# Performance work log

Measured on AMD Instinct MI355X. Metric: run time of the kernel, lower is better.

The kernel has to match this reference:

```python
import jax, jax.numpy as jnp
import numpy as np
from jax import lax

N_LAYER = 2
D_MODEL = 256
D_INNER = 512   # expand * d_model
D_STATE = 16
DT_RANK = 16    # ceil(d_model / 16)
D_CONV = 4
VOCAB = 256
B, L = 4, 2048


def setup_inputs() -> dict:
    key = jax.random.key(0)
    ks = jax.random.split(key, 12)
    s = 0.02
    embedding = jax.random.normal(ks[0], (VOCAB, D_MODEL), jnp.float32) * s
    in_proj_w = jax.random.normal(ks[1], (N_LAYER, D_MODEL, 2 * D_INNER), jnp.float32) * s
    conv_w = jax.random.normal(ks[2], (N_LAYER, D_INNER, 1, D_CONV), jnp.float32) * 0.1
    conv_b = jax.random.normal(ks[3], (N_LAYER, D_INNER), jnp.float32) * 0.01
    x_proj_w = jax.random.normal(ks[4], (N_LAYER, D_INNER, DT_RANK + 2 * D_STATE), jnp.float32) * s
    dt_proj_w = jax.random.normal(ks[5], (N_LAYER, DT_RANK, D_INNER), jnp.float32) * (DT_RANK ** -0.5)
    dt_proj_b = jax.random.normal(ks[6], (N_LAYER, D_INNER), jnp.float32) * 0.1
    # S4D-real init: A = -[1..d_state], stored as A_log
    A_log = jnp.log(jnp.broadcast_to(jnp.arange(1, D_STATE + 1, dtype=jnp.float32), (N_LAYER, D_INNER, D_STATE)))
    D = jnp.ones((N_LAYER, D_INNER), jnp.float32)
    out_proj_w = jax.random.normal(ks[7], (N_LAYER, D_INNER, D_MODEL), jnp.float32) * s
    input_ids = jax.random.randint(ks[8], (B, L), 0, VOCAB)
    return {"input_ids": input_ids, "embedding": embedding, "in_proj_w": in_proj_w,
            "conv_w": conv_w, "conv_b": conv_b, "x_proj_w": x_proj_w,
            "dt_proj_w": dt_proj_w, "dt_proj_b": dt_proj_b, "A_log": A_log,
            "D": D, "out_proj_w": out_proj_w}


def _selective_scan(u, delta, A, Bc, Cc):
    # u, delta: [B, L, d_inner]; A: [d_inner, N]; Bc, Cc: [B, L, N]
    def step(h, inp):
        d_t, b_t, c_t, u_t = inp  # [B,d_inner], [B,N], [B,N], [B,d_inner]
        dA = jnp.exp(d_t[:, :, None] * A)                    # [B, d_inner, N]
        h = dA * h + (d_t * u_t)[:, :, None] * b_t[:, None, :]
        y = jnp.sum(h * c_t[:, None, :], axis=-1)            # [B, d_inner]
        return h, y

    h0 = jnp.zeros((u.shape[0], u.shape[2], A.shape[1]), u.dtype)
    xs = (jnp.moveaxis(delta, 1, 0), jnp.moveaxis(Bc, 1, 0),
          jnp.moveaxis(Cc, 1, 0), jnp.moveaxis(u, 1, 0))
    _, ys = lax.scan(step, h0, xs)  # ys: [L, B, d_inner]
    return jnp.moveaxis(ys, 0, 1)


def _mamba_block(x, w_in, w_conv, b_conv, w_xp, w_dt, b_dt, A_log, Dp, w_out):
    # x: [B, L, d_model]
    xz = x @ w_in                                            # [B, L, 2*d_inner]
    u, res = jnp.split(xz, 2, axis=-1)
    # depthwise causal conv1d
    uc = jnp.transpose(u, (0, 2, 1))                          # [B, d_inner, L]
    uc = lax.conv_general_dilated(uc, w_conv, window_strides=(1,),
                                  padding=[(D_CONV - 1, 0)],
                                  feature_group_count=D_INNER,
                                  dimension_numbers=("NCH", "OIH", "NCH"))
    uc = uc + b_conv[None, :, None]
    u = jax.nn.silu(jnp.transpose(uc, (0, 2, 1)))             # [B, L, d_inner]
    x_dbl = u @ w_xp                                          # [B, L, dt_rank + 2N]
    dt, Bc, Cc = jnp.split(x_dbl, [DT_RANK, DT_RANK + D_STATE], axis=-1)
    delta = jax.nn.softplus(dt @ w_dt + b_dt)                 # [B, L, d_inner]
    A = -jnp.exp(A_log)                                       # [d_inner, N]
    y = _selective_scan(u, delta, A, Bc, Cc) + u * Dp
    y = y * jax.nn.silu(res)
    return y @ w_out                                          # [B, L, d_model]


def reference(input_ids, embedding, in_proj_w, conv_w, conv_b, x_proj_w,
              dt_proj_w, dt_proj_b, A_log, D, out_proj_w):
    x = embedding[input_ids]                                  # [B, L, d_model]
    for l in range(N_LAYER):
        x = _mamba_block(x, in_proj_w[l], conv_w[l], conv_b[l], x_proj_w[l],
                         dt_proj_w[l], dt_proj_b[l], A_log[l], D[l], out_proj_w[l])
    return x
```

## Files before the change

kernel.cpp:

```cpp
#include <hip/hip_runtime.h>
#include <math.h>

#define NLAYER 2
#define DMODEL 256
#define DINNER 512
#define DSTATE 16
#define DTRANK 16
#define DCONV  4
#define BB     4
#define LL     2048
#define BL     (BB*LL)
#define NCHUNK 64
#define LC     (LL/NCHUNK)
#define NREC   (BB*DINNER*DSTATE)

typedef __attribute__((ext_vector_type(8))) short short8;
typedef __attribute__((ext_vector_type(4))) float f32x4;

__device__ __forceinline__ float sigmoidf_(float x) { return 1.0f / (1.0f + __expf(-x)); }

__device__ __forceinline__ unsigned f2bf(float a) {
    unsigned u = __builtin_bit_cast(unsigned, a);
    return (u + 0x7fffu + ((u >> 16) & 1u)) >> 16;
}
__device__ __forceinline__ float bf2f(unsigned h) {
    return __builtin_bit_cast(float, h << 16);
}

template<int K, bool EMB>
__global__ __launch_bounds__(256) void k_cvt_a(const float* __restrict__ A,
                                               ushort* __restrict__ F,
                                               const int* __restrict__ ids,
                                               const float* __restrict__ emb) {
    constexpr int NKF = K / 32;
    const int t = blockIdx.x * 256 + threadIdx.x;
    const int l = t & 63;
    const int cid = t >> 6;
    const int kf = cid % NKF;
    const int mf = cid / NKF;
    const int row = mf * 16 + (l & 15);
    const int k0 = kf * 32 + (l >> 4) * 8;
    const float* src = EMB ? &emb[(size_t)ids[row] * K + k0]
                           : &A[(size_t)row * K + k0];
    float4 v0 = *(const float4*)&src[0];
    float4 v1 = *(const float4*)&src[4];
    float s[8] = {v0.x, v0.y, v0.z, v0.w, v1.x, v1.y, v1.z, v1.w};
    unsigned hi[8], lo[8];
#pragma unroll
    for (int j = 0; j < 8; ++j) {
        hi[j] = f2bf(s[j]);
        lo[j] = f2bf(s[j] - bf2f(hi[j]));
    }
    uint4 ph = make_uint4(hi[0] | (hi[1] << 16), hi[2] | (hi[3] << 16),
                          hi[4] | (hi[5] << 16), hi[6] | (hi[7] << 16));
    uint4 pl = make_uint4(lo[0] | (lo[1] << 16), lo[2] | (lo[3] << 16),
                          lo[4] | (lo[5] << 16), lo[6] | (lo[7] << 16));
    size_t ohi = ((size_t)mf * (2 * NKF) + kf) * 512 + l * 8;
    *(uint4*)&F[ohi] = ph;
    *(uint4*)&F[ohi + (size_t)NKF * 512] = pl;
}

template<int K>
__global__ __launch_bounds__(256) void k_cvt_w(const float* __restrict__ W,
                                               ushort* __restrict__ F, int N) {
    constexpr int NKF = K / 32;
    const int t = blockIdx.x * 256 + threadIdx.x;
    const int l = t & 63;
    const int cid = t >> 6;
    const int kf = cid % NKF;
    const int nf = cid / NKF;
    const int col = nf * 16 + (l & 15);
    const int k0 = kf * 32 + (l >> 4) * 8;
    float s[8];
#pragma unroll
    for (int j = 0; j < 8; ++j) s[j] = W[(size_t)(k0 + j) * N + col];
    unsigned hi[8], lo[8];
#pragma unroll
    for (int j = 0; j < 8; ++j) {
        hi[j] = f2bf(s[j]);
        lo[j] = f2bf(s[j] - bf2f(hi[j]));
    }
    uint4 ph = make_uint4(hi[0] | (hi[1] << 16), hi[2] | (hi[3] << 16),
                          hi[4] | (hi[5] << 16), hi[6] | (hi[7] << 16));
    uint4 pl = make_uint4(lo[0] | (lo[1] << 16), lo[2] | (lo[3] << 16),
                          lo[4] | (lo[5] << 16), lo[6] | (lo[7] << 16));
    size_t ohi = ((size_t)nf * (2 * NKF) + kf) * 512 + l * 8;
    *(uint4*)&F[ohi] = ph;
    *(uint4*)&F[ohi + (size_t)NKF * 512] = pl;
}

template<int SPLITK>
__global__ __launch_bounds__(256) void k_mgemm(const ushort* __restrict__ Af,
                                               const ushort* __restrict__ Bf,
                                               float* __restrict__ C,
                                               int M, int N, int KE) {
    __shared__ __align__(16) ushort As[8 * 512];
    __shared__ __align__(16) ushort Bs[8 * 512];
    const int tid = threadIdx.x;
    const int w = tid >> 6, lane = tid & 63;
    const int n0 = blockIdx.x * 128, m0 = blockIdx.y * 128;
    const int nkf = KE >> 5;
    const int KT = nkf / SPLITK;
    const int kt0 = blockIdx.z * KT;
    const int wm = w & 1, wn = w >> 1;
    const int c0 = 2 * w, c1 = c0 + 1;

    f32x4 acc[4][4] = {};

    const ushort* Ab0 = Af + ((size_t)(m0 / 16 + c0) * nkf) * 512 + lane * 8;
    const ushort* Ab1 = Af + ((size_t)(m0 / 16 + c1) * nkf) * 512 + lane * 8;
    const ushort* Bb0 = Bf + ((size_t)(n0 / 16 + c0) * nkf) * 512 + lane * 8;
    const ushort* Bb1 = Bf + ((size_t)(n0 / 16 + c1) * nkf) * 512 + lane * 8;
    ushort* As0 = As + c0 * 512 + lane * 8;
    ushort* As1 = As + c1 * 512 + lane * 8;
    ushort* Bs0 = Bs + c0 * 512 + lane * 8;
    ushort* Bs1 = Bs + c1 * 512 + lane * 8;

    for (int kt = kt0; kt < kt0 + KT; ++kt) {
        const size_t ko = (size_t)kt * 512;
        __builtin_amdgcn_global_load_lds((const __attribute__((address_space(1))) void*)(Ab0 + ko),
                                         (__attribute__((address_space(3))) void*)As0, 16, 0, 0);
        __builtin_amdgcn_global_load_lds((const __attribute__((address_space(1))) void*)(Ab1 + ko),
                                         (__attribute__((address_space(3))) void*)As1, 16, 0, 0);
        __builtin_amdgcn_global_load_lds((const __attribute__((address_space(1))) void*)(Bb0 + ko),
                                         (__attribute__((address_space(3))) void*)Bs0, 16, 0, 0);
        __builtin_amdgcn_global_load_lds((const __attribute__((address_space(1))) void*)(Bb1 + ko),
                                         (__attribute__((address_space(3))) void*)Bs1, 16, 0, 0);
        __syncthreads();
        short8 av[4], bv[4];
#pragma unroll
        for (int i = 0; i < 4; ++i)
            av[i] = *(const short8*)&As[(wm * 4 + i) * 512 + lane * 8];
#pragma unroll
        for (int i = 0; i < 4; ++i)
            bv[i] = *(const short8*)&Bs[(wn * 4 + i) * 512 + lane * 8];
#pragma unroll
        for (int mi = 0; mi < 4; ++mi)
#pragma unroll
            for (int ni = 0; ni < 4; ++ni)
                acc[mi][ni] = __builtin_amdgcn_mfma_f32_16x16x32_bf16(av[mi], bv[ni],
                                                                      acc[mi][ni], 0, 0, 0);
        __syncthreads();
    }

    float* Cw = C + (size_t)blockIdx.z * ((size_t)M * N);
    const int r0 = (lane >> 4) * 4, cc = lane & 15;
#pragma unroll
    for (int mi = 0; mi < 4; ++mi)
#pragma unroll
        for (int r = 0; r < 4; ++r) {
            const int row = m0 + wm * 64 + mi * 16 + r0 + r;
            float* crow = &Cw[(size_t)row * N + n0 + wn * 64 + cc];
#pragma unroll
            for (int ni = 0; ni < 4; ++ni) crow[ni * 16] = acc[mi][ni][r];
        }
}

__global__ __launch_bounds__(256) void k_red4(const float* __restrict__ p,
                                              float* __restrict__ o, int n4) {
    int i = blockIdx.x * 256 + threadIdx.x;
    const float4* p4 = (const float4*)p;
    float4 a = p4[i], b = p4[i + n4], c = p4[i + 2 * n4], d = p4[i + 3 * n4];
    ((float4*)o)[i] = make_float4(a.x + b.x + c.x + d.x, a.y + b.y + c.y + d.y,
                                  a.z + b.z + c.z + d.z, a.w + b.w + c.w + d.w);
}

__global__ void k_conv_silu(const float* __restrict__ xz, const float* __restrict__ cw,
                            const float* __restrict__ cb, float* __restrict__ u) {
    int idx = blockIdx.x * blockDim.x + threadIdx.x;
    int c  = idx & (DINNER - 1);
    int bl = idx >> 9;
    int l  = bl & (LL - 1);
    float acc = cb[c];
#pragma unroll
    for (int k = 0; k < DCONV; ++k) {
        int t = l - (DCONV - 1) + k;
        if (t >= 0) acc += cw[c * DCONV + k] * xz[(size_t)(bl - (DCONV - 1) + k) * 2 * DINNER + c];
    }
    u[(size_t)idx] = acc * sigmoidf_(acc);
}

__global__ __launch_bounds__(256) void k_xpd(const float* __restrict__ u,
                                             const float* __restrict__ w_xp,
                                             const float* __restrict__ w_dt,
                                             const float* __restrict__ b_dt,
                                             float* __restrict__ Bm,
                                             float* __restrict__ Cm,
                                             float* __restrict__ delta) {
    const int tid = threadIdx.x;
    const int bl0 = blockIdx.x * 16;
    __shared__ float us[16 * DINNER];
    __shared__ float wsx[128 * 48];
    __shared__ float dts[16][DTRANK];

    {
        const float4* u4 = (const float4*)&u[(size_t)bl0 * DINNER];
        float4* us4 = (float4*)us;
#pragma unroll
        for (int q = 0; q < 8; ++q) us4[tid + q * 256] = u4[tid + q * 256];
    }

    const int mp = tid >> 5;
    const int jg = (tid >> 3) & 3;
    const int s  = tid & 7;
    const float* usm0 = &us[(mp * 2 + 0) * DINNER];
    const float* usm1 = &us[(mp * 2 + 1) * DINNER];

    float acc0[12] = {}, acc1[12] = {};
#pragma unroll 1
    for (int ck = 0; ck < 4; ++ck) {
        __syncthreads();
        {
            const float4* wg = (const float4*)&w_xp[ck * 128 * 48];
            float4* wl = (float4*)wsx;
#pragma unroll
            for (int q = 0; q < 6; ++q) wl[tid + q * 256] = wg[tid + q * 256];
        }
        __syncthreads();
#pragma unroll
        for (int i = 0; i < 16; ++i) {
            const int kl = i * 8 + s;
            const float a0 = usm0[ck * 128 + kl];
            const float a1 = usm1[ck * 128 + kl];
            const float* wr = &wsx[kl * 48 + jg * 12];
            float4 w0 = *(const float4*)&wr[0];
            float4 w1 = *(const float4*)&wr[4];
            float4 w2 = *(const float4*)&wr[8];
            acc0[0]  = fmaf(a0, w0.x, acc0[0]);  acc1[0]  = fmaf(a1, w0.x, acc1[0]);
            acc0[1]  = fmaf(a0, w0.y, acc0[1]);  acc1[1]  = fmaf(a1, w0.y, acc1[1]);
            acc0[2]  = fmaf(a0, w0.z, acc0[2]);  acc1[2]  = fmaf(a1, w0.z, acc1[2]);
            acc0[3]  = fmaf(a0, w0.w, acc0[3]);  acc1[3]  = fmaf(a1, w0.w, acc1[3]);
            acc0[4]  = fmaf(a0, w1.x, acc0[4]);  acc1[4]  = fmaf(a1, w1.x, acc1[4]);
            acc0[5]  = fmaf(a0, w1.y, acc0[5]);  acc1[5]  = fmaf(a1, w1.y, acc1[5]);
            acc0[6]  = fmaf(a0, w1.z, acc0[6]);  acc1[6]  = fmaf(a1, w1.z, acc1[6]);
            acc0[7]  = fmaf(a0, w1.w, acc0[7]);  acc1[7]  = fmaf(a1, w1.w, acc1[7]);
            acc0[8]  = fmaf(a0, w2.x, acc0[8]);  acc1[8]  = fmaf(a1, w2.x, acc1[8]);
            acc0[9]  = fmaf(a0, w2.y, acc0[9]);  acc1[9]  = fmaf(a1, w2.y, acc1[9]);
            acc0[10] = fmaf(a0, w2.z, acc0[10]); acc1[10] = fmaf(a1, w2.z, acc1[10]);
            acc0[11] = fmaf(a0, w2.w, acc0[11]); acc1[11] = fmaf(a1, w2.w, acc1[11]);
        }
    }
#pragma unroll
    for (int off = 4; off >= 1; off >>= 1) {
#pragma unroll
        for (int j = 0; j < 12; ++j) {
            acc0[j] += __shfl_xor(acc0[j], off, 8);
            acc1[j] += __shfl_xor(acc1[j], off, 8);
        }
    }
    if (s < 6) {
        const int bl_a = bl0 + mp * 2 + 0;
        const int bl_b = bl0 + mp * 2 + 1;
#pragma unroll
        for (int q = 0; q < 2; ++q) {
            int j = jg * 12 + s * 2 + q;
            float v0 = acc0[s * 2 + q];
            float v1 = acc1[s * 2 + q];
            if (j < 16) {
                dts[mp * 2 + 0][j] = v0;
                dts[mp * 2 + 1][j] = v1;
            } else if (j < 32) {
                Bm[(size_t)bl_a * DSTATE + (j - 16)] = v0;
                Bm[(size_t)bl_b * DSTATE + (j - 16)] = v1;
            } else {
                Cm[(size_t)bl_a * DSTATE + (j - 32)] = v0;
                Cm[(size_t)bl_b * DSTATE + (j - 32)] = v1;
            }
        }
    }
    __syncthreads();

    const int c0 = (tid & 127) * 4;
    const int mb = (tid >> 7) * 8;
    float4 bd = *(const float4*)&b_dt[c0];
    float a0[8], a1[8], a2[8], a3[8];
#pragma unroll
    for (int t = 0; t < 8; ++t) { a0[t] = bd.x; a1[t] = bd.y; a2[t] = bd.z; a3[t] = bd.w; }
#pragma unroll
    for (int r = 0; r < DTRANK; ++r) {
        float4 w4 = *(const float4*)&w_dt[r * DINNER + c0];
#pragma unroll
        for (int t = 0; t < 8; ++t) {
            float f = dts[mb + t][r];
            a0[t] = fmaf(f, w4.x, a0[t]);
            a1[t] = fmaf(f, w4.y, a1[t]);
            a2[t] = fmaf(f, w4.z, a2[t]);
            a3[t] = fmaf(f, w4.w, a3[t]);
        }
    }
#pragma unroll
    for (int t = 0; t < 8; ++t) {
        float4 o;
        o.x = (a0[t] > 20.f) ? a0[t] : log1pf(__expf(a0[t]));
        o.y = (a1[t] > 20.f) ? a1[t] : log1pf(__expf(a1[t]));
        o.z = (a2[t] > 20.f) ? a2[t] : log1pf(__expf(a2[t]));
        o.w = (a3[t] > 20.f) ? a3[t] : log1pf(__expf(a3[t]));
        *(float4*)&delta[(size_t)(bl0 + mb + t) * DINNER + c0] = o;
    }
}

__global__ __launch_bounds__(256) void k_scan_a(const float* __restrict__ delta,
                                                const float* __restrict__ u,
                                                const float* __restrict__ Bm,
                                                const float* __restrict__ A_log,
                                                float* __restrict__ aprod,
                                                float* __restrict__ hend) {
    const int tid = threadIdx.x;
    const int bid = blockIdx.x;
    const int chalf = bid & 1;
    const int k = (bid >> 1) & (NCHUNK - 1);
    const int b = bid >> 7;
    const int c = chalf * 256 + tid;
    const int bl0 = b * LL + k * LC;

    __shared__ float Bs[LC * DSTATE];
    for (int i = tid; i < LC * DSTATE; i += 256) Bs[i] = Bm[(size_t)bl0 * DSTATE + i];
    __syncthreads();

    float Ac[DSTATE];
#pragma unroll
    for (int q = 0; q < 4; ++q) {
        float4 a = *(const float4*)&A_log[c * DSTATE + q * 4];
        Ac[q * 4 + 0] = -__expf(a.x); Ac[q * 4 + 1] = -__expf(a.y);
        Ac[q * 4 + 2] = -__expf(a.z); Ac[q * 4 + 3] = -__expf(a.w);
    }

    float h[DSTATE] = {};
    float ap[DSTATE];
#pragma unroll
    for (int n = 0; n < DSTATE; ++n) ap[n] = 1.f;

    float dlt = delta[(size_t)bl0 * DINNER + c];
    float uu  = u[(size_t)bl0 * DINNER + c];
    for (int t = 0; t < LC; ++t) {
        float dlt2 = 0.f, uu2 = 0.f;
        if (t + 1 < LC) {
            dlt2 = delta[(size_t)(bl0 + t + 1) * DINNER + c];
            uu2  = u[(size_t)(bl0 + t + 1) * DINNER + c];
        }
        const float w = dlt * uu;
        const float4* Bs4 = (const float4*)&Bs[t * DSTATE];
        float4 b0 = Bs4[0], b1 = Bs4[1], b2 = Bs4[2], b3 = Bs4[3];
        float bv[DSTATE] = {b0.x, b0.y, b0.z, b0.w, b1.x, b1.y, b1.z, b1.w,
                            b2.x, b2.y, b2.z, b2.w, b3.x, b3.y, b3.z, b3.w};
#pragma unroll
        for (int n = 0; n < DSTATE; ++n) {
            float dA = __expf(dlt * Ac[n]);
            ap[n] *= dA;
            h[n] = fmaf(dA, h[n], w * bv[n]);
        }
        dlt = dlt2; uu = uu2;
    }
    size_t base = ((size_t)(k * BB + b) * DINNER + c) * DSTATE;
#pragma unroll
    for (int q = 0; q < 4; ++q) {
        *(float4*)&aprod[base + q * 4] = make_float4(ap[q*4], ap[q*4+1], ap[q*4+2], ap[q*4+3]);
        *(float4*)&hend[base + q * 4]  = make_float4(h[q*4],  h[q*4+1],  h[q*4+2],  h[q*4+3]);
    }
}

__global__ __launch_bounds__(256) void k_scan_b(const float* __restrict__ aprod,
                                                const float* __restrict__ hend,
                                                float* __restrict__ hstart) {
    int i = blockIdx.x * 256 + threadIdx.x;
    float h = 0.f;
#pragma unroll 4
    for (int k = 0; k < NCHUNK; ++k) {
        size_t idx = (size_t)k * NREC + i;
        float a = aprod[idx];
        float e = hend[idx];
        hstart[idx] = h;
        h = fmaf(a, h, e);
    }
}

__global__ __launch_bounds__(256) void k_scan_c(const float* __restrict__ delta,
                                                const float* __restrict__ u,
                                                const float* __restrict__ xz,
                                                const float* __restrict__ Bm,
                                                const float* __restrict__ Cm,
                                                const float* __restrict__ A_log,
                                                const float* __restrict__ Dp,
                                                const float* __restrict__ hstart,
                                                float* __restrict__ y) {
    const int tid = threadIdx.x;
    const int bid = blockIdx.x;
    const int chalf = bid & 1;
    const int k = (bid >> 1) & (NCHUNK - 1);
    const int b = bid >> 7;
    const int c = chalf * 256 + tid;
    const int bl0 = b * LL + k * LC;

    __shared__ float Bs[LC * DSTATE];
    __shared__ float Cs[LC * DSTATE];
    for (int i = tid; i < LC * DSTATE; i += 256) {
        Bs[i] = Bm[(size_t)bl0 * DSTATE + i];
        Cs[i] = Cm[(size_t)bl0 * DSTATE + i];
    }
    __syncthreads();

    float Ac[DSTATE];
#pragma unroll
    for (int q = 0; q < 4; ++q) {
        float4 a = *(const float4*)&A_log[c * DSTATE + q * 4];
        Ac[q * 4 + 0] = -__expf(a.x); Ac[q * 4 + 1] = -__expf(a.y);
        Ac[q * 4 + 2] = -__expf(a.z); Ac[q * 4 + 3] = -__expf(a.w);
    }
    const float Dc = Dp[c];

    float h[DSTATE];
    size_t hbase = ((size_t)(k * BB + b) * DINNER + c) * DSTATE;
#pragma unroll
    for (int q = 0; q < 4; ++q) {
        float4 hv = *(const float4*)&hstart[hbase + q * 4];
        h[q*4] = hv.x; h[q*4+1] = hv.y; h[q*4+2] = hv.z; h[q*4+3] = hv.w;
    }

    float dlt = delta[(size_t)bl0 * DINNER + c];
    float uu  = u[(size_t)bl0 * DINNER + c];
    float rr  = xz[(size_t)bl0 * 2 * DINNER + DINNER + c];
    for (int t = 0; t < LC; ++t) {
        float dlt2 = 0.f, uu2 = 0.f, rr2 = 0.f;
        if (t + 1 < LC) {
            dlt2 = delta[(size_t)(bl0 + t + 1) * DINNER + c];
            uu2  = u[(size_t)(bl0 + t + 1) * DINNER + c];
            rr2  = xz[(size_t)(bl0 + t + 1) * 2 * DINNER + DINNER + c];
        }
        const float w = dlt * uu;
        const float4* Bs4 = (const float4*)&Bs[t * DSTATE];
        float4 b0 = Bs4[0], b1 = Bs4[1], b2 = Bs4[2], b3 = Bs4[3];
        float bv[DSTATE] = {b0.x, b0.y, b0.z, b0.w, b1.x, b1.y, b1.z, b1.w,
                            b2.x, b2.y, b2.z, b2.w, b3.x, b3.y, b3.z, b3.w};
        const float4* Cs4 = (const float4*)&Cs[t * DSTATE];
        float4 c0 = Cs4[0], c1 = Cs4[1], c2 = Cs4[2], c3 = Cs4[3];
        float cv[DSTATE] = {c0.x, c0.y, c0.z, c0.w, c1.x, c1.y, c1.z, c1.w,
                            c2.x, c2.y, c2.z, c2.w, c3.x, c3.y, c3.z, c3.w};
        float s0 = 0.f, s1 = 0.f, s2 = 0.f, s3 = 0.f;
#pragma unroll
        for (int n = 0; n < DSTATE; n += 4) {
            float dA0 = __expf(dlt * Ac[n+0]);
            float dA1 = __expf(dlt * Ac[n+1]);
            float dA2 = __expf(dlt * Ac[n+2]);
            float dA3 = __expf(dlt * Ac[n+3]);
            h[n+0] = fmaf(dA0, h[n+0], w * bv[n+0]);
            h[n+1] = fmaf(dA1, h[n+1], w * bv[n+1]);
            h[n+2] = fmaf(dA2, h[n+2], w * bv[n+2]);
            h[n+3] = fmaf(dA3, h[n+3], w * bv[n+3]);
            s0 = fmaf(h[n+0], cv[n+0], s0);
            s1 = fmaf(h[n+1], cv[n+1], s1);
            s2 = fmaf(h[n+2], cv[n+2], s2);
            s3 = fmaf(h[n+3], cv[n+3], s3);
        }
        float yv = (s0 + s1) + (s2 + s3) + uu * Dc;
        y[(size_t)(bl0 + t) * DINNER + c] = yv * (rr * sigmoidf_(rr));
        dlt = dlt2; uu = uu2; rr = rr2;
    }
}

extern "C" void kernel_launch(void* const* d_in, const int* in_sizes, int n_in,
                              void* d_out, int out_size, void* d_ws, size_t ws_size,
                              hipStream_t stream) {
    const int*   ids   = (const int*)d_in[0];
    const float* emb   = (const float*)d_in[1];
    const float* w_in  = (const float*)d_in[2];
    const float* cw    = (const float*)d_in[3];
    const float* cb    = (const float*)d_in[4];
    const float* w_xp  = (const float*)d_in[5];
    const float* w_dt  = (const float*)d_in[6];
    const float* b_dt  = (const float*)d_in[7];
    const float* A_log = (const float*)d_in[8];
    const float* Dp    = (const float*)d_in[9];
    const float* w_out = (const float*)d_in[10];
    float* out = (float*)d_out;

    float* ws = (float*)d_ws;
    float* x    = ws;
    float* xz   = x  + (size_t)BL * DMODEL;
    float* u    = xz + (size_t)BL * 2 * DINNER;
    float* Bm   = u  + (size_t)BL * DINNER;
    float* Cm   = Bm + (size_t)BL * DSTATE;
    float* dlt  = Cm + (size_t)BL * DSTATE;
    float* y    = dlt + (size_t)BL * DINNER;
    float* hend = y + (size_t)BL * DINNER;
    float* wfif = hend + (size_t)NCHUNK * NREC;
    float* wfof = wfif + 262144;
    float* aprod  = x;
    float* hstart = aprod;
    ushort* xfrag = (ushort*)hend;
    ushort* yfrag = (ushort*)u;
    ushort* wfi = (ushort*)wfif;
    ushort* wfo = (ushort*)wfof;

    for (int l = 0; l < NLAYER; ++l) {
        if (l == 0)
            k_cvt_a<DMODEL, true><<<1024, 256, 0, stream>>>(x, xfrag, ids, emb);
        else
            k_cvt_a<DMODEL, false><<<1024, 256, 0, stream>>>(x, xfrag, ids, emb);
        k_cvt_w<DMODEL><<<128, 256, 0, stream>>>(w_in + (size_t)l * DMODEL * 2 * DINNER,
                                                 wfi, 2 * DINNER);
        k_mgemm<1><<<dim3(2 * DINNER / 128, BL / 128, 1), 256, 0, stream>>>(
            xfrag, wfi, xz, BL, 2 * DINNER, 2 * DMODEL);

        k_conv_silu<<<(BL * DINNER) / 256, 256, 0, stream>>>(
            xz, cw + l * DINNER * DCONV, cb + l * DINNER, u);
        k_xpd<<<BL / 16, 256, 0, stream>>>(u, w_xp + (size_t)l * DINNER * 48,
                                           w_dt + (size_t)l * DTRANK * DINNER,
                                           b_dt + (size_t)l * DINNER, Bm, Cm, dlt);
        const float* Al = A_log + (size_t)l * DINNER * DSTATE;
        k_scan_a<<<BB * NCHUNK * 2, 256, 0, stream>>>(dlt, u, Bm, Al, aprod, hend);
        k_scan_b<<<NREC / 256, 256, 0, stream>>>(aprod, hend, hstart);
        k_scan_c<<<BB * NCHUNK * 2, 256, 0, stream>>>(dlt, u, xz, Bm, Cm, Al,
                                                      Dp + (size_t)l * DINNER, hstart, y);

        k_cvt_a<DINNER, false><<<2048, 256, 0, stream>>>(y, yfrag, ids, emb);
        k_cvt_w<DINNER><<<64, 256, 0, stream>>>(w_out + (size_t)l * DINNER * DMODEL,
                                                wfo, DMODEL);
        float* dst = (l == NLAYER - 1) ? out : x;
        k_mgemm<4><<<dim3(DMODEL / 128, BL / 128, 4), 256, 0, stream>>>(
            yfrag, wfo, xz, BL, DMODEL, 2 * DINNER);
        k_red4<<<(BL * DMODEL / 4) / 256, 256, 0, stream>>>(xz, dst, BL * DMODEL / 4);
    }
}
```

Measured before the change: 335.7 us.

## Fuse bf16 split conversions into producers and gather embedding rows in GEMM

Drops the separate activation-to-fragment conversion kernels. Producers (the scan output stage and the split-K reduction) now write hi/lo bf16 row-major data directly. The first GEMM gathers embedding rows by token id from a pre-converted embedding table. The depthwise conv+SiLU is also fused into the x-projection kernel, removing a kernel and a round trip through u. The cost is that GEMM A loads change from a contiguous fragment layout to row-strided 16-byte loads, which may coalesce worse.

```diff
diff --git a/kernel.cpp b/kernel.cpp
--- a/kernel.cpp
+++ b/kernel.cpp
@@ -13,6 +13,7 @@
 #define NCHUNK 64
 #define LC     (LL/NCHUNK)
 #define NREC   (BB*DINNER*DSTATE)
+#define VOCAB  256
 
 typedef __attribute__((ext_vector_type(8))) short short8;
 typedef __attribute__((ext_vector_type(4))) float f32x4;
@@ -27,37 +28,15 @@
     return __builtin_bit_cast(float, h << 16);
 }
 
-template<int K, bool EMB>
-__global__ __launch_bounds__(256) void k_cvt_a(const float* __restrict__ A,
-                                               ushort* __restrict__ F,
-                                               const int* __restrict__ ids,
-                                               const float* __restrict__ emb) {
-    constexpr int NKF = K / 32;
-    const int t = blockIdx.x * 256 + threadIdx.x;
-    const int l = t & 63;
-    const int cid = t >> 6;
-    const int kf = cid % NKF;
-    const int mf = cid / NKF;
-    const int row = mf * 16 + (l & 15);
-    const int k0 = kf * 32 + (l >> 4) * 8;
-    const float* src = EMB ? &emb[(size_t)ids[row] * K + k0]
-                           : &A[(size_t)row * K + k0];
-    float4 v0 = *(const float4*)&src[0];
-    float4 v1 = *(const float4*)&src[4];
-    float s[8] = {v0.x, v0.y, v0.z, v0.w, v1.x, v1.y, v1.z, v1.w};
-    unsigned hi[8], lo[8];
-#pragma unroll
-    for (int j = 0; j < 8; ++j) {
-        hi[j] = f2bf(s[j]);
-        lo[j] = f2bf(s[j] - bf2f(hi[j]));
-    }
-    uint4 ph = make_uint4(hi[0] | (hi[1] << 16), hi[2] | (hi[3] << 16),
-                          hi[4] | (hi[5] << 16), hi[6] | (hi[7] << 16));
-    uint4 pl = make_uint4(lo[0] | (lo[1] << 16), lo[2] | (lo[3] << 16),
-                          lo[4] | (lo[5] << 16), lo[6] | (lo[7] << 16));
-    size_t ohi = ((size_t)mf * (2 * NKF) + kf) * 512 + l * 8;
-    *(uint4*)&F[ohi] = ph;
-    *(uint4*)&F[ohi + (size_t)NKF * 512] = pl;
+__global__ __launch_bounds__(256) void k_cvt_emb(const float* __restrict__ emb,
+                                                 ushort* __restrict__ embf) {
+    const int v = blockIdx.x;
+    const int c = threadIdx.x;
+    float s = emb[(size_t)v * DMODEL + c];
+    unsigned hi = f2bf(s);
+    unsigned lo = f2bf(s - bf2f(hi));
+    embf[(size_t)v * (2 * DMODEL) + c] = (ushort)hi;
+    embf[(size_t)v * (2 * DMODEL) + DMODEL + c] = (ushort)lo;
 }
 
 template<int K>
@@ -89,11 +68,12 @@
     *(uint4*)&F[ohi + (size_t)NKF * 512] = pl;
 }
 
-template<int SPLITK>
-__global__ __launch_bounds__(256) void k_mgemm(const ushort* __restrict__ Af,
+template<int SPLITK, bool IDS>
+__global__ __launch_bounds__(256) void k_mgemm(const ushort* __restrict__ A,
                                                const ushort* __restrict__ Bf,
                                                float* __restrict__ C,
-                                               int M, int N, int KE) {
+                                               int M, int N, int KE,
+                                               const int* __restrict__ ids) {
     __shared__ __align__(16) ushort As[8 * 512];
     __shared__ __align__(16) ushort Bs[8 * 512];
     const int tid = threadIdx.x;
@@ -107,8 +87,11 @@
 
     f32x4 acc[4][4] = {};
 
-    const ushort* Ab0 = Af + ((size_t)(m0 / 16 + c0) * nkf) * 512 + lane * 8;
-    const ushort* Ab1 = Af + ((size_t)(m0 / 16 + c1) * nkf) * 512 + lane * 8;
+    int row0 = m0 + c0 * 16 + (lane & 15);
+    int row1 = m0 + c1 * 16 + (lane & 15);
+    if (IDS) { row0 = ids[row0]; row1 = ids[row1]; }
+    const ushort* Ap0 = A + (size_t)row0 * KE + (lane >> 4) * 8;
+    const ushort* Ap1 = A + (size_t)row1 * KE + (lane >> 4) * 8;
     const ushort* Bb0 = Bf + ((size_t)(n0 / 16 + c0) * nkf) * 512 + lane * 8;
     const ushort* Bb1 = Bf + ((size_t)(n0 / 16 + c1) * nkf) * 512 + lane * 8;
     ushort* As0 = As + c0 * 512 + lane * 8;
@@ -117,14 +100,13 @@
     ushort* Bs1 = Bs + c1 * 512 + lane * 8;
 
     for (int kt = kt0; kt < kt0 + KT; ++kt) {
-        const size_t ko = (size_t)kt * 512;
-        __builtin_amdgcn_global_load_lds((const __attribute__((address_space(1))) void*)(Ab0 + ko),
+        __builtin_amdgcn_global_load_lds((const __attribute__((address_space(1))) void*)(Ap0 + kt * 32),
                                          (__attribute__((address_space(3))) void*)As0, 16, 0, 0);
-        __builtin_amdgcn_global_load_lds((const __attribute__((address_space(1))) void*)(Ab1 + ko),
+        __builtin_amdgcn_global_load_lds((const __attribute__((address_space(1))) void*)(Ap1 + kt * 32),
                                          (__attribute__((address_space(3))) void*)As1, 16, 0, 0);
-        __builtin_amdgcn_global_load_lds((const __attribute__((address_space(1))) void*)(Bb0 + ko),
+        __builtin_amdgcn_global_load_lds((const __attribute__((address_space(1))) void*)(Bb0 + (size_t)kt * 512),
                                          (__attribute__((address_space(3))) void*)Bs0, 16, 0, 0);
-        __builtin_amdgcn_global_load_lds((const __attribute__((address_space(1))) void*)(Bb1 + ko),
+        __builtin_amdgcn_global_load_lds((const __attribute__((address_space(1))) void*)(Bb1 + (size_t)kt * 512),
                                          (__attribute__((address_space(3))) void*)Bs1, 16, 0, 0);
         __syncthreads();
         short8 av[4], bv[4];
@@ -156,34 +138,42 @@
         }
 }
 
+template<bool TOBF>
 __global__ __launch_bounds__(256) void k_red4(const float* __restrict__ p,
-                                              float* __restrict__ o, int n4) {
+                                              float* __restrict__ o,
+                                              ushort* __restrict__ xb, int n4) {
     int i = blockIdx.x * 256 + threadIdx.x;
     const float4* p4 = (const float4*)p;
     float4 a = p4[i], b = p4[i + n4], c = p4[i + 2 * n4], d = p4[i + 3 * n4];
-    ((float4*)o)[i] = make_float4(a.x + b.x + c.x + d.x, a.y + b.y + c.y + d.y,
-                                  a.z + b.z + c.z + d.z, a.w + b.w + c.w + d.w);
-}
-
-__global__ void k_conv_silu(const float* __restrict__ xz, const float* __restrict__ cw,
-                            const float* __restrict__ cb, float* __restrict__ u) {
-    int idx = blockIdx.x * blockDim.x + threadIdx.x;
-    int c  = idx & (DINNER - 1);
-    int bl = idx >> 9;
-    int l  = bl & (LL - 1);
-    float acc = cb[c];
-#pragma unroll
-    for (int k = 0; k < DCONV; ++k) {
-        int t = l - (DCONV - 1) + k;
-        if (t >= 0) acc += cw[c * DCONV + k] * xz[(size_t)(bl - (DCONV - 1) + k) * 2 * DINNER + c];
-    }
-    u[(size_t)idx] = acc * sigmoidf_(acc);
-}
-
-__global__ __launch_bounds__(256) void k_xpd(const float* __restrict__ u,
+    float4 r = make_float4(a.x + b.x + c.x + d.x, a.y + b.y + c.y + d.y,
+                           a.z + b.z + c.z + d.z, a.w + b.w + c.w + d.w);
+    if (TOBF) {
+        const int e0 = i * 4;
+        const int bl = e0 >> 8;
+        const int cl = e0 & 255;
+        float s[4] = {r.x, r.y, r.z, r.w};
+        unsigned hi[4], lo[4];
+#pragma unroll
+        for (int j = 0; j < 4; ++j) {
+            hi[j] = f2bf(s[j]);
+            lo[j] = f2bf(s[j] - bf2f(hi[j]));
+        }
+        *(uint2*)&xb[(size_t)bl * 512 + cl] =
+            make_uint2(hi[0] | (hi[1] << 16), hi[2] | (hi[3] << 16));
+        *(uint2*)&xb[(size_t)bl * 512 + 256 + cl] =
+            make_uint2(lo[0] | (lo[1] << 16), lo[2] | (lo[3] << 16));
+    } else {
+        ((float4*)o)[i] = r;
+    }
+}
+
+__global__ __launch_bounds__(256) void k_xpd(const float* __restrict__ xz,
+                                             const float* __restrict__ cw,
+                                             const float* __restrict__ cb,
                                              const float* __restrict__ w_xp,
                                              const float* __restrict__ w_dt,
                                              const float* __restrict__ b_dt,
+                                             float* __restrict__ u,
                                              float* __restrict__ Bm,
                                              float* __restrict__ Cm,
                                              float* __restrict__ delta) {
@@ -194,10 +184,32 @@
     __shared__ float dts[16][DTRANK];
 
     {
-        const float4* u4 = (const float4*)&u[(size_t)bl0 * DINNER];
-        float4* us4 = (float4*)us;
-#pragma unroll
-        for (int q = 0; q < 8; ++q) us4[tid + q * 256] = u4[tid + q * 256];
+        const int ch0 = tid, ch1 = 256 + tid;
+        float4 cwA = *(const float4*)&cw[ch0 * 4];
+        float4 cwB = *(const float4*)&cw[ch1 * 4];
+        const float cbA = cb[ch0], cbB = cb[ch1];
+        const int lbase = bl0 & (LL - 1);
+#pragma unroll
+        for (int m = 0; m < 16; ++m) {
+            const int bl = bl0 + m;
+            const int lpos = lbase + m;
+            float aA = cbA, aB = cbB;
+#pragma unroll
+            for (int k = 0; k < DCONV; ++k) {
+                int tt = lpos - (DCONV - 1) + k;
+                if (tt >= 0) {
+                    const float* xr = &xz[(size_t)(bl - (DCONV - 1) + k) * 2 * DINNER];
+                    aA = fmaf(((const float*)&cwA)[k], xr[ch0], aA);
+                    aB = fmaf(((const float*)&cwB)[k], xr[ch1], aB);
+                }
+            }
+            float uA = aA * sigmoidf_(aA);
+            float uB = aB * sigmoidf_(aB);
+            us[m * DINNER + ch0] = uA;
+            us[m * DINNER + ch1] = uB;
+            u[(size_t)bl * DINNER + ch0] = uA;
+            u[(size_t)bl * DINNER + ch1] = uB;
+        }
     }
 
     const int mp = tid >> 5;
@@ -382,7 +394,7 @@
                                                 const float* __restrict__ A_log,
                                                 const float* __restrict__ Dp,
                                                 const float* __restrict__ hstart,
-                                                float* __restrict__ y) {
+                                                ushort* __restrict__ yb) {
     const int tid = threadIdx.x;
     const int bid = blockIdx.x;
     const int chalf = bid & 1;
@@ -452,7 +464,11 @@
             s3 = fmaf(h[n+3], cv[n+3], s3);
         }
         float yv = (s0 + s1) + (s2 + s3) + uu * Dc;
-        y[(size_t)(bl0 + t) * DINNER + c] = yv * (rr * sigmoidf_(rr));
+        float yg = yv * (rr * sigmoidf_(rr));
+        unsigned hi = f2bf(yg);
+        unsigned lo = f2bf(yg - bf2f(hi));
+        yb[(size_t)(bl0 + t) * (2 * DINNER) + c] = (ushort)hi;
+        yb[(size_t)(bl0 + t) * (2 * DINNER) + DINNER + c] = (ushort)lo;
         dlt = dlt2; uu = uu2; rr = rr2;
     }
 }
@@ -484,40 +500,47 @@
     float* hend = y + (size_t)BL * DINNER;
     float* wfif = hend + (size_t)NCHUNK * NREC;
     float* wfof = wfif + 262144;
+    float* embff = wfof + 131072;
     float* aprod  = x;
     float* hstart = aprod;
-    ushort* xfrag = (ushort*)hend;
-    ushort* yfrag = (ushort*)u;
-    ushort* wfi = (ushort*)wfif;
-    ushort* wfo = (ushort*)wfof;
+    ushort* xb   = (ushort*)x;
+    ushort* yb   = (ushort*)y;
+    ushort* wfi  = (ushort*)wfif;
+    ushort* wfo  = (ushort*)wfof;
+    ushort* embf = (ushort*)embff;
+
+    k_cvt_emb<<<VOCAB, DMODEL, 0, stream>>>(emb, embf);
 
     for (int l = 0; l < NLAYER; ++l) {
-        if (l == 0)
-            k_cvt_a<DMODEL, true><<<1024, 256, 0, stream>>>(x, xfrag, ids, emb);
-        else
-            k_cvt_a<DMODEL, false><<<1024, 256, 0, stream>>>(x, xfrag, ids, emb);
         k_cvt_w<DMODEL><<<128, 256, 0, stream>>>(w_in + (size_t)l * DMODEL * 2 * DINNER,
                                                  wfi, 2 * DINNER);
-        k_mgemm<1><<<dim3(2 * DINNER / 128, BL / 128, 1), 256, 0, stream>>>(
-            xfrag, wfi, xz, BL, 2 * DINNER, 2 * DMODEL);
-
-        k_conv_silu<<<(BL * DINNER) / 256, 256, 0, stream>>>(
-            xz, cw + l * DINNER * DCONV, cb + l * DINNER, u);
-        k_xpd<<<BL / 16, 256, 0, stream>>>(u, w_xp + (size_t)l * DINNER * 48,
+        if (l == 0)
+            k_mgemm<1, true><<<dim3(2 * DINNER / 128, BL / 128, 1), 256, 0, stream>>>(
+                embf, wfi, xz, BL, 2 * DINNER, 2 * DMODEL, ids);
+        else
+            k_mgemm<1, false><<<dim3(2 * DINNER / 128, BL / 128, 1), 256, 0, stream>>>(
+                xb, wfi, xz, BL, 2 * DINNER, 2 * DMODEL, ids);
+
+        k_xpd<<<BL / 16, 256, 0, stream>>>(xz, cw + l * DINNER * DCONV, cb + l * DINNER,
+                                           w_xp + (size_t)l * DINNER * 48,
                                            w_dt + (size_t)l * DTRANK * DINNER,
-                                           b_dt + (size_t)l * DINNER, Bm, Cm, dlt);
+                                           b_dt + (size_t)l * DINNER, u, Bm, Cm, dlt);
+
         const float* Al = A_log + (size_t)l * DINNER * DSTATE;
         k_scan_a<<<BB * NCHUNK * 2, 256, 0, stream>>>(dlt, u, Bm, Al, aprod, hend);
         k_scan_b<<<NREC / 256, 256, 0, stream>>>(aprod, hend, hstart);
         k_scan_c<<<BB * NCHUNK * 2, 256, 0, stream>>>(dlt, u, xz, Bm, Cm, Al,
-                                                      Dp + (size_t)l * DINNER, hstart, y);
-
-        k_cvt_a<DINNER, false><<<2048, 256, 0, stream>>>(y, yfrag, ids, emb);
+                                                      Dp + (size_t)l * DINNER, hstart, yb);
+
         k_cvt_w<DINNER><<<64, 256, 0, stream>>>(w_out + (size_t)l * DINNER * DMODEL,
                                                 wfo, DMODEL);
-        float* dst = (l == NLAYER - 1) ? out : x;
-        k_mgemm<4><<<dim3(DMODEL / 128, BL / 128, 4), 256, 0, stream>>>(
-            yfrag, wfo, xz, BL, DMODEL, 2 * DINNER);
-        k_red4<<<(BL * DMODEL / 4) / 256, 256, 0, stream>>>(xz, dst, BL * DMODEL / 4);
-    }
-}
+        k_mgemm<4, false><<<dim3(DMODEL / 128, BL / 128, 4), 256, 0, stream>>>(
+            yb, wfo, xz, BL, DMODEL, 2 * DINNER, ids);
+        if (l == NLAYER - 1)
+            k_red4<false><<<(BL * DMODEL / 4) / 256, 256, 0, stream>>>(xz, out, xb,
+                                                                       BL * DMODEL / 4);
+        else
+            k_red4<true><<<(BL * DMODEL / 4) / 256, 256, 0, stream>>>(xz, out, xb,
+                                                                      BL * DMODEL / 4);
+    }
+}
```

Result: faster. 288.5 us, median of 2 (-14.1%).
